# Optimization experiments

Hardware: AMD Instinct MI355X
Metric: run time of the kernel (lower is better)

The kernel has to match this reference:

```python
import jax, jax.numpy as jnp
import numpy as np

EPS = 1e-12


def _l2norm(x):
    # F.normalize(x, dim=1): x / max(||x||, eps)
    n = jnp.sqrt(jnp.sum(x * x, axis=1, keepdims=True))
    return x / jnp.maximum(n, EPS)


def _remove_diag(x):
    # x: [n, n] -> [n, n-1], dropping the diagonal (matches x[~eye].view(n, -1))
    n = x.shape[0]
    row = jnp.arange(n)[:, None]
    base = jnp.arange(n - 1)[None, :]
    cols = jnp.where(base < row, base, base + 1)  # column indices != row index
    return jnp.take_along_axis(x, cols, axis=1)


def _lid_mle(data, reference, k):
    # pairwise euclidean distances [n_data, n_ref]
    d2 = (jnp.sum(data * data, axis=1)[:, None]
          + jnp.sum(reference * reference, axis=1)[None, :]
          - 2.0 * data @ reference.T)
    dist = jnp.sqrt(jnp.maximum(d2, 0.0))
    # k+1 smallest distances (index 0 is the self-distance since data subset of reference)
    neg_top, _ = jax.lax.top_k(-dist, k + 1)
    d = -neg_top[:, 1:]  # [n, k], ascending, self excluded
    # MLE LID estimator: -k / sum_i log(d_i / d_k)
    return -k / jnp.sum(jnp.log(d / d[:, -1:] + EPS), axis=1)


def _byol_loss(p, z):
    z = jax.lax.stop_gradient(z)
    return 2.0 - 2.0 * jnp.sum(_l2norm(p) * _l2norm(z), axis=1)


def _track_logits(o0, o1):
    b = o0.shape[0]
    l00 = _remove_diag(jnp.einsum('nc,mc->nm', o0, o0))
    l01 = jnp.einsum('nc,mc->nm', o0, o1)
    l10 = jnp.einsum('nc,mc->nm', o1, o0)
    l11 = _remove_diag(jnp.einsum('nc,mc->nm', o1, o1))
    logits = jnp.concatenate([
        jnp.concatenate([l01, l00], axis=1),
        jnp.concatenate([l10, l11], axis=1)], axis=0)  # [2b, 2b-1]
    labels = jnp.tile(jnp.arange(b, dtype=jnp.int32), 2)
    return logits, labels


def setup_inputs() -> dict:
    key = jax.random.key(0)
    ks = jax.random.split(key, 9)
    B, Dfe, Dp, C = 4096, 2048, 256, 1000
    return {
        'fe_0': jax.random.normal(ks[0], (B, Dfe), jnp.float32),
        'fe_1': jax.random.normal(ks[1], (B, Dfe), jnp.float32),
        'p_0': jax.random.normal(ks[2], (B, Dp), jnp.float32),
        'p_1': jax.random.normal(ks[3], (B, Dp), jnp.float32),
        'z_0': jax.random.normal(ks[4], (B, Dp), jnp.float32),
        'z_1': jax.random.normal(ks[5], (B, Dp), jnp.float32),
        'cls_0': jax.random.normal(ks[6], (B, C), jnp.float32),
        'cls_1': jax.random.normal(ks[7], (B, C), jnp.float32),
        'online_labels': jax.random.randint(ks[8], (B,), 0, C, jnp.int32),
    }


def reference(fe_0, fe_1, p_0, p_1, z_0, z_1, cls_0, cls_1, online_labels):
    # BYOL symmetric loss
    main_loss = jnp.mean(_byol_loss(p_0, z_1) + _byol_loss(p_1, z_0))
    # online linear-probe cross-entropy on concatenated views
    cls = jnp.concatenate([cls_0, cls_1], axis=0)
    labels2 = jnp.concatenate([online_labels, online_labels], axis=0)
    logp = jax.nn.log_softmax(cls, axis=1)
    online_loss = -jnp.mean(jnp.take_along_axis(logp, labels2[:, None], axis=1)[:, 0])
    # LID tracking on backbone features (no-grad in original)
    fe = jnp.concatenate([fe_0, fe_1], axis=0)
    lids32 = _lid_mle(fe, fe, 32)
    lids512 = _lid_mle(fe, fe, 512)
    # contrastive-style logit tracking on normalized predictor outputs
    logits, labels = _track_logits(_l2norm(p_0), _l2norm(p_1))
    return main_loss, online_loss, logits, labels, lids32, lids512
```

## Files before the change

kernel.cpp:

```cpp
#include <hip/hip_runtime.h>
#include <math.h>

typedef __bf16 bf16;
typedef __bf16 bf16x8 __attribute__((ext_vector_type(8)));
typedef __bf16 bf16x4 __attribute__((ext_vector_type(4)));
typedef float f32x4 __attribute__((ext_vector_type(4)));

#define NROW 8192
#define BHALF 4096
#define DFE 2048
#define DP 256
#define NCLS 1000

#define LOGITS_N 8191
#define OUT_LOGITS 2
#define OUT_LABELS (2 + 8192 * 8191)
#define OUT_LIDS32 (OUT_LABELS + 8192)
#define OUT_LIDS512 (OUT_LIDS32 + 8192)

#define G0TILES 1056
#define G1TILES 2048

__device__ inline void gload16(const bf16* g, bf16* l) {
    __builtin_amdgcn_global_load_lds((const __attribute__((address_space(1))) void*)g,
                                     (__attribute__((address_space(3))) void*)l, 16, 0, 0);
}

__global__ __launch_bounds__(256) void init_kernel(float* out) {
    int i = blockIdx.x * 256 + threadIdx.x;
    if (i < 2) out[i] = 0.f;
    if (i < NROW) out[(size_t)OUT_LABELS + i] = (float)(i & (BHALF - 1));
}

__global__ __launch_bounds__(256) void split_fe_kernel(const float* __restrict__ fe0,
                                                       const float* __restrict__ fe1,
                                                       bf16* __restrict__ feh,
                                                       bf16* __restrict__ fel,
                                                       float* __restrict__ norms) {
    int row = blockIdx.x, tid = threadIdx.x;
    const float* src = (row < BHALF) ? fe0 + (size_t)row * DFE
                                     : fe1 + (size_t)(row - BHALF) * DFE;
    float ss = 0.f;
#pragma unroll
    for (int pass = 0; pass < 2; ++pass) {
        int c = (pass * 256 + tid) * 4;
        float4 v = *(const float4*)(src + c);
        ss += v.x * v.x + v.y * v.y + v.z * v.z + v.w * v.w;
        bf16 h0 = (bf16)v.x, h1 = (bf16)v.y, h2 = (bf16)v.z, h3 = (bf16)v.w;
        bf16 l0 = (bf16)(v.x - (float)h0), l1 = (bf16)(v.y - (float)h1);
        bf16 l2 = (bf16)(v.z - (float)h2), l3 = (bf16)(v.w - (float)h3);
        bf16x4 hv = {h0, h1, h2, h3};
        bf16x4 lv = {l0, l1, l2, l3};
        *(bf16x4*)(feh + (size_t)row * DFE + c) = hv;
        *(bf16x4*)(fel + (size_t)row * DFE + c) = lv;
    }
#pragma unroll
    for (int off = 32; off; off >>= 1) ss += __shfl_down(ss, off);
    __shared__ float red[4];
    if ((tid & 63) == 0) red[tid >> 6] = ss;
    __syncthreads();
    if (tid == 0) norms[row] = red[0] + red[1] + red[2] + red[3];
}

__global__ __launch_bounds__(256) void norm_split_p_kernel(const float* __restrict__ p0,
                                                           const float* __restrict__ p1,
                                                           bf16* __restrict__ oh) {
    int row = blockIdx.x, tid = threadIdx.x;
    const float* src = (row < BHALF) ? p0 + (size_t)row * DP
                                     : p1 + (size_t)(row - BHALF) * DP;
    float x = src[tid];
    float ss = x * x;
#pragma unroll
    for (int off = 32; off; off >>= 1) ss += __shfl_down(ss, off);
    __shared__ float red[4];
    if ((tid & 63) == 0) red[tid >> 6] = ss;
    __syncthreads();
    float tot = red[0] + red[1] + red[2] + red[3];
    float rn = 1.f / fmaxf(sqrtf(tot), 1e-12f);
    oh[(size_t)row * DP + tid] = (bf16)(x * rn);
}

__device__ inline float dot4(float4 a, float4 b) {
    return a.x * b.x + a.y * b.y + a.z * b.z + a.w * b.w;
}

__global__ __launch_bounds__(256) void byol_kernel(const float* __restrict__ p0,
                                                   const float* __restrict__ p1,
                                                   const float* __restrict__ z0,
                                                   const float* __restrict__ z1,
                                                   float* out) {
    int tid = threadIdx.x, wave = tid >> 6, lane = tid & 63;
    int row = blockIdx.x * 4 + wave;
    size_t base = (size_t)row * DP + lane * 4;
    float4 a0 = *(const float4*)(p0 + base);
    float4 b0 = *(const float4*)(z1 + base);
    float4 a1 = *(const float4*)(p1 + base);
    float4 b1 = *(const float4*)(z0 + base);
    float pp0 = dot4(a0, a0), zz0 = dot4(b0, b0), pz0 = dot4(a0, b0);
    float pp1 = dot4(a1, a1), zz1 = dot4(b1, b1), pz1 = dot4(a1, b1);
#pragma unroll
    for (int off = 32; off; off >>= 1) {
        pp0 += __shfl_down(pp0, off); zz0 += __shfl_down(zz0, off); pz0 += __shfl_down(pz0, off);
        pp1 += __shfl_down(pp1, off); zz1 += __shfl_down(zz1, off); pz1 += __shfl_down(pz1, off);
    }
    __shared__ float red[4];
    if (lane == 0) {
        float c0 = pz0 / (fmaxf(sqrtf(pp0), 1e-12f) * fmaxf(sqrtf(zz0), 1e-12f));
        float c1 = pz1 / (fmaxf(sqrtf(pp1), 1e-12f) * fmaxf(sqrtf(zz1), 1e-12f));
        red[wave] = (2.f - 2.f * c0) + (2.f - 2.f * c1);
    }
    __syncthreads();
    if (tid == 0) atomicAdd(out, (red[0] + red[1] + red[2] + red[3]) * (1.f / 4096.f));
}

__global__ __launch_bounds__(256) void online_kernel(const float* __restrict__ cls0,
                                                     const float* __restrict__ cls1,
                                                     const int* __restrict__ labels,
                                                     float* out) {
    int tid = threadIdx.x, wave = tid >> 6, lane = tid & 63;
    int row = blockIdx.x * 4 + wave;
    const float* src = (row < BHALF) ? cls0 + (size_t)row * NCLS
                                     : cls1 + (size_t)(row - BHALF) * NCLS;
    int lbl = labels[row & (BHALF - 1)];
    float xs[16];
    float mx = -INFINITY;
#pragma unroll
    for (int j = 0; j < 16; ++j) {
        int c = lane + j * 64;
        xs[j] = (c < NCLS) ? src[c] : -INFINITY;
        mx = fmaxf(mx, xs[j]);
    }
#pragma unroll
    for (int off = 32; off; off >>= 1) mx = fmaxf(mx, __shfl_xor(mx, off));
    float se = 0.f;
#pragma unroll
    for (int j = 0; j < 16; ++j) se += expf(xs[j] - mx);
#pragma unroll
    for (int off = 32; off; off >>= 1) se += __shfl_xor(se, off);
    __shared__ float red[4];
    if (lane == 0) red[wave] = src[lbl] - mx - logf(se);
    __syncthreads();
    if (tid == 0) atomicAdd(out + 1, -(red[0] + red[1] + red[2] + red[3]) * (1.f / 8192.f));
}

__global__ __launch_bounds__(512, 2) void gemm_kernel(const bf16* __restrict__ Hp,
                                                      const bf16* __restrict__ Lp,
                                                      const bf16* __restrict__ OHp,
                                                      const float* __restrict__ norms,
                                                      float* __restrict__ d2,
                                                      float* __restrict__ outlog) {
    __shared__ bf16 sm[2][24576];
    int tid = threadIdx.x, lane = tid & 63, wave = tid >> 6;
    int wr = wave >> 1, wc = wave & 1;
    int lrow = lane & 15, lquad = lane >> 4, r7 = lrow & 7, pg = lquad ^ r7;
    int rsub = lane >> 3, grp = lane & 7, lg = grp ^ rsub;

    int bid = blockIdx.x;
    int mode, tm, tn, ksh;
    const bf16 *Hmat, *Lmat;
    int Kd;
    if (bid < G0TILES) {
        mode = 0;
        int sw = (bid & 7) * (G0TILES / 8) + (bid >> 3);
        int i = 0;
        while ((i + 1) * (65 - (i + 1)) <= sw) ++i;
        tm = i;
        tn = 2 * i + (sw - i * (65 - i));
        Hmat = Hp; Lmat = Lp; Kd = DFE; ksh = 5;
    } else {
        mode = 1;
        int id = bid - G0TILES;
        int sw = (id & 7) * (G1TILES / 8) + (id >> 3);
        tm = sw & 31; tn = sw >> 5;
        Hmat = OHp; Lmat = OHp; Kd = DP; ksh = 2;
    }
    int NT = (mode == 0 ? 3 : 1) << ksh;
    int kmask = (1 << ksh) - 1;
    int arow0 = tm * 256, brow0 = tn * 128;
    size_t delta = (size_t)(Lmat - Hmat);

    const bf16* baseA[4];
    const bf16* baseB[2];
#pragma unroll
    for (int q = 0; q < 4; ++q)
        baseA[q] = Hmat + (size_t)(arow0 + q * 64 + wave * 8 + rsub) * Kd + lg * 8;
#pragma unroll
    for (int q = 0; q < 2; ++q)
        baseB[q] = Hmat + (size_t)(brow0 + q * 64 + wave * 8 + rsub) * Kd + lg * 8;

    int aoff[4], boff[4];
#pragma unroll
    for (int t = 0; t < 4; ++t) {
        aoff[t] = (((t * 4 + wr) * 16 + lrow) * 64) * 2 + pg * 16;
        boff[t] = 32768 + (((t * 2 + wc) * 16 + lrow) * 64) * 2 + pg * 16;
    }
    const char* S0 = (const char*)sm[0];
    const char* S1 = (const char*)sm[1];

    f32x4 acc[4][4];
    f32x4 zz = {0.f, 0.f, 0.f, 0.f};
#pragma unroll
    for (int i = 0; i < 4; ++i)
#pragma unroll
        for (int j = 0; j < 4; ++j) acc[i][j] = zz;

#define STAGE(nt, B)                                                        \
    do {                                                                    \
        int ch_ = (nt) >> ksh;                                              \
        int k_ = ((nt) & kmask) << 6;                                       \
        size_t dA_ = (ch_ == 1) ? delta : 0;                                \
        size_t dB_ = (ch_ == 2) ? delta : 0;                                \
        _Pragma("unroll") for (int q = 0; q < 4; ++q)                       \
            gload16(baseA[q] + dA_ + k_, (B) + q * 4096 + wave * 512);      \
        _Pragma("unroll") for (int q = 0; q < 2; ++q)                       \
            gload16(baseB[q] + dB_ + k_, (B) + 16384 + q * 4096 + wave * 512); \
    } while (0)

#define READF(AF, BF, SB)                                                   \
    do {                                                                    \
        _Pragma("unroll") for (int t = 0; t < 4; ++t) {                     \
            AF[t][0] = *(const bf16x8*)((SB) + aoff[t]);                    \
            AF[t][1] = *(const bf16x8*)((SB) + (aoff[t] ^ 64));             \
        }                                                                   \
        _Pragma("unroll") for (int t = 0; t < 4; ++t) {                     \
            BF[t][0] = *(const bf16x8*)((SB) + boff[t]);                    \
            BF[t][1] = *(const bf16x8*)((SB) + (boff[t] ^ 64));             \
        }                                                                   \
    } while (0)

#define MFMAC(AF, BF)                                                       \
    do {                                                                    \
        __builtin_amdgcn_s_setprio(1);                                      \
        _Pragma("unroll") for (int i = 0; i < 4; ++i)                       \
            _Pragma("unroll") for (int j = 0; j < 4; ++j) {                 \
                acc[i][j] = __builtin_amdgcn_mfma_f32_16x16x32_bf16(AF[i][0], BF[j][0], acc[i][j], 0, 0, 0); \
                acc[i][j] = __builtin_amdgcn_mfma_f32_16x16x32_bf16(AF[i][1], BF[j][1], acc[i][j], 0, 0, 0); \
            }                                                               \
        __builtin_amdgcn_s_setprio(0);                                      \
    } while (0)

    bf16x8 af0[4][2], bf0[4][2], af1[4][2], bf1[4][2];

    STAGE(0, sm[0]);
    STAGE(1, sm[1]);
    asm volatile("s_waitcnt vmcnt(6)" ::: "memory");
    __builtin_amdgcn_s_barrier();
    __builtin_amdgcn_sched_barrier(0);
    READF(af0, bf0, S0);

    for (int t = 0; t < NT; t += 2) {
        asm volatile("s_waitcnt lgkmcnt(0)" ::: "memory");
        __builtin_amdgcn_sched_barrier(0);
        __builtin_amdgcn_s_barrier();
        if (t + 2 < NT) {
            STAGE(t + 2, sm[0]);
            asm volatile("s_waitcnt vmcnt(6)" ::: "memory");
        } else {
            asm volatile("s_waitcnt vmcnt(0)" ::: "memory");
        }
        __builtin_amdgcn_s_barrier();
        __builtin_amdgcn_sched_barrier(0);
        READF(af1, bf1, S1);
        __builtin_amdgcn_sched_barrier(0);
        MFMAC(af0, bf0);

        asm volatile("s_waitcnt lgkmcnt(0)" ::: "memory");
        __builtin_amdgcn_sched_barrier(0);
        __builtin_amdgcn_s_barrier();
        if (t + 3 < NT) {
            STAGE(t + 3, sm[1]);
            asm volatile("s_waitcnt vmcnt(6)" ::: "memory");
        } else if (t + 2 < NT) {
            asm volatile("s_waitcnt vmcnt(0)" ::: "memory");
        }
        __builtin_amdgcn_s_barrier();
        if (t + 2 < NT) {
            __builtin_amdgcn_sched_barrier(0);
            READF(af0, bf0, S0);
            __builtin_amdgcn_sched_barrier(0);
        }
        MFMAC(af1, bf1);
    }

    if (mode == 0) {
#pragma unroll
        for (int i = 0; i < 4; ++i) {
#pragma unroll
            for (int e = 0; e < 4; ++e) {
                int grow = arow0 + (i * 4 + wr) * 16 + lquad * 4 + e;
                float na = norms[grow];
#pragma unroll
                for (int j = 0; j < 4; ++j) {
                    int gcol = tn * 128 + (j * 2 + wc) * 16 + lrow;
                    float v = na + norms[gcol] - 2.f * acc[i][j][e];
                    d2[(size_t)grow * NROW + gcol] = fmaxf(v, 0.f);
                }
            }
        }
    } else {
#pragma unroll
        for (int i = 0; i < 4; ++i) {
#pragma unroll
            for (int j = 0; j < 4; ++j) {
#pragma unroll
                for (int e = 0; e < 4; ++e) {
                    int r = arow0 + (i * 4 + wr) * 16 + lquad * 4 + e;
                    int c = tn * 128 + (j * 2 + wc) * 16 + lrow;
                    int oc = 0;
                    bool skip = false;
                    if (r < BHALF) {
                        if (c >= BHALF) oc = c - BHALF;
                        else if (c == r) skip = true;
                        else oc = BHALF + (c < r ? c : c - 1);
                    } else {
                        int rp = r - BHALF;
                        if (c < BHALF) oc = c;
                        else {
                            int cp = c - BHALF;
                            if (cp == rp) skip = true;
                            else oc = BHALF + (cp < rp ? cp : cp - 1);
                        }
                    }
                    if (!skip) outlog[(size_t)r * LOGITS_N + oc] = acc[i][j][e];
                }
            }
        }
    }
#undef STAGE
#undef READF
#undef MFMAC
}

__global__ __launch_bounds__(256) void mirror_kernel(float* __restrict__ d2) {
    int bj = blockIdx.x, bi = blockIdx.y;
    if (bi < bj) return;
    __shared__ float t[32][33];
    int tx = threadIdx.x & 31, ty = threadIdx.x >> 5;
#pragma unroll
    for (int r = 0; r < 32; r += 8)
        t[r + ty][tx] = d2[(size_t)(bj * 32 + r + ty) * NROW + bi * 32 + tx];
    __syncthreads();
#pragma unroll
    for (int r = 0; r < 32; r += 8) {
        int gi = bi * 32 + r + ty, gj = bj * 32 + tx;
        if (gi > gj) d2[(size_t)gi * NROW + gj] = t[tx][r + ty];
    }
}

__global__ __launch_bounds__(256) void select_kernel(const float* __restrict__ d2,
                                                     float* __restrict__ out) {
    int wave = threadIdx.x >> 6, lane = threadIdx.x & 63;
    int row = blockIdx.x * 4 + wave;
    const float4* drow4 = (const float4*)(d2 + (size_t)row * NROW);
    unsigned v[128];
    unsigned andv = 0xFFFFFFFFu, orv = 0u;
#pragma unroll
    for (int j = 0; j < 32; ++j) {
        int idx4 = j * 64 + lane;
        float4 f = drow4[idx4];
        int c0 = idx4 * 4;
        unsigned u0 = __float_as_uint(f.x), u1 = __float_as_uint(f.y);
        unsigned u2 = __float_as_uint(f.z), u3 = __float_as_uint(f.w);
        bool s0 = (c0 == row), s1 = (c0 + 1 == row), s2 = (c0 + 2 == row), s3 = (c0 + 3 == row);
        v[j * 4 + 0] = s0 ? 0xFFFFFFFFu : u0;
        v[j * 4 + 1] = s1 ? 0xFFFFFFFFu : u1;
        v[j * 4 + 2] = s2 ? 0xFFFFFFFFu : u2;
        v[j * 4 + 3] = s3 ? 0xFFFFFFFFu : u3;
        andv &= (s0 ? 0xFFFFFFFFu : u0); orv |= (s0 ? 0u : u0);
        andv &= (s1 ? 0xFFFFFFFFu : u1); orv |= (s1 ? 0u : u1);
        andv &= (s2 ? 0xFFFFFFFFu : u2); orv |= (s2 ? 0u : u2);
        andv &= (s3 ? 0xFFFFFFFFu : u3); orv |= (s3 ? 0u : u3);
    }
#pragma unroll
    for (int off = 32; off; off >>= 1) {
        andv &= __shfl_xor(andv, off);
        orv |= __shfl_xor(orv, off);
    }
    unsigned diff = andv ^ orv;
    int msb = 31 - __clz((int)(diff | 1u));
    unsigned common = (msb == 31) ? 0u : (andv & (0xFFFFFFFFu << (msb + 1)));
    unsigned p1 = common, p2 = common;
    for (int bit = msb; bit >= 0; --bit) {
        unsigned c1 = p1 | (1u << bit), c2 = p2 | (1u << bit);
        unsigned n1 = 0, n2 = 0;
#pragma unroll
        for (int j = 0; j < 128; ++j) { n1 += (v[j] < c1); n2 += (v[j] < c2); }
#pragma unroll
        for (int off = 32; off; off >>= 1) {
            n1 += __shfl_xor(n1, off);
            n2 += __shfl_xor(n2, off);
        }
        if (n1 < 32u) p1 = c1;
        if (n2 < 512u) p2 = c2;
    }
    float dk1 = sqrtf(__uint_as_float(p1));
    float dk2 = sqrtf(__uint_as_float(p2));
    float s1 = 0.f, s2 = 0.f;
#pragma unroll
    for (int j = 0; j < 128; ++j) {
        unsigned b = v[j];
        if (b < p2) {
            float d = sqrtf(__uint_as_float(b));
            s2 += logf(d / dk2 + 1e-12f);
            if (b < p1) s1 += logf(d / dk1 + 1e-12f);
        }
    }
#pragma unroll
    for (int off = 32; off; off >>= 1) {
        s1 += __shfl_xor(s1, off);
        s2 += __shfl_xor(s2, off);
    }
    if (lane == 0) {
        out[(size_t)OUT_LIDS32 + row] = -32.f / s1;
        out[(size_t)OUT_LIDS512 + row] = -512.f / s2;
    }
}

extern "C" void kernel_launch(void* const* d_in, const int* in_sizes, int n_in,
                              void* d_out, int out_size, void* d_ws, size_t ws_size,
                              hipStream_t stream) {
    const float* fe0 = (const float*)d_in[0];
    const float* fe1 = (const float*)d_in[1];
    const float* p0 = (const float*)d_in[2];
    const float* p1 = (const float*)d_in[3];
    const float* z0 = (const float*)d_in[4];
    const float* z1 = (const float*)d_in[5];
    const float* cls0 = (const float*)d_in[6];
    const float* cls1 = (const float*)d_in[7];
    const int* labels = (const int*)d_in[8];
    float* out = (float*)d_out;

    char* ws = (char*)d_ws;
    float* D2 = (float*)ws;
    bf16* FEH = (bf16*)(ws + 268435456UL);
    bf16* FEL = (bf16*)(ws + 268435456UL + 33554432UL);
    bf16* OH = (bf16*)(ws + 268435456UL + 2 * 33554432UL);
    float* NORMS = (float*)(ws + 268435456UL + 2 * 33554432UL + 4194304UL);

    init_kernel<<<32, 256, 0, stream>>>(out);
    split_fe_kernel<<<8192, 256, 0, stream>>>(fe0, fe1, FEH, FEL, NORMS);
    norm_split_p_kernel<<<8192, 256, 0, stream>>>(p0, p1, OH);
    byol_kernel<<<1024, 256, 0, stream>>>(p0, p1, z0, z1, out);
    online_kernel<<<2048, 256, 0, stream>>>(cls0, cls1, labels, out);
    gemm_kernel<<<G0TILES + G1TILES, 512, 0, stream>>>(FEH, FEL, OH, NORMS, D2, out + OUT_LOGITS);
    mirror_kernel<<<dim3(256, 256), 256, 0, stream>>>(D2);
    select_kernel<<<2048, 256, 0, stream>>>(D2, out);
}
```

Measured before the change: 1.252 ms.

## Enlarge GEMM tiles to 256x256 with quarter-phase pipelined staging; widen mirror tiles

```diff
diff --git a/kernel.cpp b/kernel.cpp
--- a/kernel.cpp
+++ b/kernel.cpp
@@ -18,8 +18,8 @@
 #define OUT_LIDS32 (OUT_LABELS + 8192)
 #define OUT_LIDS512 (OUT_LIDS32 + 8192)
 
-#define G0TILES 1056
-#define G1TILES 2048
+#define G0TILES 528
+#define G1TILES 1024
 
 __device__ inline void gload16(const bf16* g, bf16* l) {
     __builtin_amdgcn_global_load_lds((const __attribute__((address_space(1))) void*)g,
@@ -149,9 +149,9 @@
                                                       const float* __restrict__ norms,
                                                       float* __restrict__ d2,
                                                       float* __restrict__ outlog) {
-    __shared__ bf16 sm[2][24576];
+    __shared__ bf16 sm[2][32768];
     int tid = threadIdx.x, lane = tid & 63, wave = tid >> 6;
-    int wr = wave >> 1, wc = wave & 1;
+    int wr = wave >> 2, wn = wave & 3;
     int lrow = lane & 15, lquad = lane >> 4, r7 = lrow & 7, pg = lquad ^ r7;
     int rsub = lane >> 3, grp = lane & 7, lg = grp ^ rsub;
 
@@ -163,9 +163,9 @@
         mode = 0;
         int sw = (bid & 7) * (G0TILES / 8) + (bid >> 3);
         int i = 0;
-        while ((i + 1) * (65 - (i + 1)) <= sw) ++i;
+        while ((i + 1) * (64 - i) / 2 <= sw) ++i;
         tm = i;
-        tn = 2 * i + (sw - i * (65 - i));
+        tn = tm + (sw - i * (65 - i) / 2);
         Hmat = Hp; Lmat = Lp; Kd = DFE; ksh = 5;
     } else {
         mode = 1;
@@ -176,122 +176,147 @@
     }
     int NT = (mode == 0 ? 3 : 1) << ksh;
     int kmask = (1 << ksh) - 1;
-    int arow0 = tm * 256, brow0 = tn * 128;
+    int arow0 = tm * 256, brow0 = tn * 256;
     size_t delta = (size_t)(Lmat - Hmat);
 
-    const bf16* baseA[4];
-    const bf16* baseB[2];
-#pragma unroll
-    for (int q = 0; q < 4; ++q)
-        baseA[q] = Hmat + (size_t)(arow0 + q * 64 + wave * 8 + rsub) * Kd + lg * 8;
-#pragma unroll
-    for (int q = 0; q < 2; ++q)
-        baseB[q] = Hmat + (size_t)(brow0 + q * 64 + wave * 8 + rsub) * Kd + lg * 8;
-
-    int aoff[4], boff[4];
-#pragma unroll
-    for (int t = 0; t < 4; ++t) {
-        aoff[t] = (((t * 4 + wr) * 16 + lrow) * 64) * 2 + pg * 16;
-        boff[t] = 32768 + (((t * 2 + wc) * 16 + lrow) * 64) * 2 + pg * 16;
-    }
-    const char* S0 = (const char*)sm[0];
-    const char* S1 = (const char*)sm[1];
-
-    f32x4 acc[4][4];
+    const bf16* baseA0 = Hmat + (size_t)(arow0 + wave * 8 + rsub) * Kd + lg * 8;
+    const bf16* baseB0 = Hmat + (size_t)(brow0 + wave * 8 + rsub) * Kd + lg * 8;
+
+    int aoffbase[2], boffbase[2];
+    aoffbase[0] = (wr * 64 + lrow) * 128 + pg * 16;
+    aoffbase[1] = aoffbase[0] + 128 * 128;
+    boffbase[0] = 32768 + (wn * 32 + lrow) * 128 + pg * 16;
+    boffbase[1] = boffbase[0] + 128 * 128;
+
+    f32x4 acc[8][4];
     f32x4 zz = {0.f, 0.f, 0.f, 0.f};
 #pragma unroll
-    for (int i = 0; i < 4; ++i)
+    for (int i = 0; i < 8; ++i)
 #pragma unroll
         for (int j = 0; j < 4; ++j) acc[i][j] = zz;
 
-#define STAGE(nt, B)                                                        \
-    do {                                                                    \
-        int ch_ = (nt) >> ksh;                                              \
-        int k_ = ((nt) & kmask) << 6;                                       \
-        size_t dA_ = (ch_ == 1) ? delta : 0;                                \
-        size_t dB_ = (ch_ == 2) ? delta : 0;                                \
-        _Pragma("unroll") for (int q = 0; q < 4; ++q)                       \
-            gload16(baseA[q] + dA_ + k_, (B) + q * 4096 + wave * 512);      \
-        _Pragma("unroll") for (int q = 0; q < 2; ++q)                       \
-            gload16(baseB[q] + dB_ + k_, (B) + 16384 + q * 4096 + wave * 512); \
-    } while (0)
-
-#define READF(AF, BF, SB)                                                   \
-    do {                                                                    \
-        _Pragma("unroll") for (int t = 0; t < 4; ++t) {                     \
-            AF[t][0] = *(const bf16x8*)((SB) + aoff[t]);                    \
-            AF[t][1] = *(const bf16x8*)((SB) + (aoff[t] ^ 64));             \
-        }                                                                   \
-        _Pragma("unroll") for (int t = 0; t < 4; ++t) {                     \
-            BF[t][0] = *(const bf16x8*)((SB) + boff[t]);                    \
-            BF[t][1] = *(const bf16x8*)((SB) + (boff[t] ^ 64));             \
-        }                                                                   \
-    } while (0)
-
-#define MFMAC(AF, BF)                                                       \
-    do {                                                                    \
-        __builtin_amdgcn_s_setprio(1);                                      \
-        _Pragma("unroll") for (int i = 0; i < 4; ++i)                       \
-            _Pragma("unroll") for (int j = 0; j < 4; ++j) {                 \
-                acc[i][j] = __builtin_amdgcn_mfma_f32_16x16x32_bf16(AF[i][0], BF[j][0], acc[i][j], 0, 0, 0); \
-                acc[i][j] = __builtin_amdgcn_mfma_f32_16x16x32_bf16(AF[i][1], BF[j][1], acc[i][j], 0, 0, 0); \
-            }                                                               \
-        __builtin_amdgcn_s_setprio(0);                                      \
-    } while (0)
-
-    bf16x8 af0[4][2], bf0[4][2], af1[4][2], bf1[4][2];
-
-    STAGE(0, sm[0]);
-    STAGE(1, sm[1]);
-    asm volatile("s_waitcnt vmcnt(6)" ::: "memory");
+#define STAGE_A(tau, h, dstbuf)                                                   \
+    do {                                                                          \
+        int tau_ = (tau);                                                         \
+        if (tau_ < NT) {                                                          \
+            int ch_ = tau_ >> ksh;                                                \
+            size_t dd_ = (ch_ == 1) ? delta : 0;                                  \
+            int k_ = (tau_ & kmask) << 6;                                         \
+            bf16* d_ = (dstbuf) + (h) * 8192 + wave * 512;                        \
+            gload16(baseA0 + (size_t)((h) * 128) * Kd + dd_ + k_, d_);            \
+            gload16(baseA0 + (size_t)((h) * 128 + 64) * Kd + dd_ + k_, d_ + 4096);\
+        }                                                                         \
+    } while (0)
+
+#define STAGE_B(tau, h, dstbuf)                                                   \
+    do {                                                                          \
+        int tau_ = (tau);                                                         \
+        if (tau_ < NT) {                                                          \
+            int ch_ = tau_ >> ksh;                                                \
+            size_t dd_ = (ch_ == 2) ? delta : 0;                                  \
+            int k_ = (tau_ & kmask) << 6;                                         \
+            bf16* d_ = (dstbuf) + 16384 + (h) * 8192 + wave * 512;                \
+            gload16(baseB0 + (size_t)((h) * 128) * Kd + dd_ + k_, d_);            \
+            gload16(baseB0 + (size_t)((h) * 128 + 64) * Kd + dd_ + k_, d_ + 4096);\
+        }                                                                         \
+    } while (0)
+
+#define READ_A(AF, MI)                                                            \
+    do {                                                                          \
+        _Pragma("unroll") for (int f = 0; f < 4; ++f) {                           \
+            int off_ = aoffbase[(MI)] + f * 2048;                                 \
+            AF[f][0] = *(const bf16x8*)(Sb + off_);                               \
+            AF[f][1] = *(const bf16x8*)(Sb + (off_ ^ 64));                        \
+        }                                                                         \
+    } while (0)
+
+#define READ_B(BF, NI)                                                            \
+    do {                                                                          \
+        _Pragma("unroll") for (int jj = 0; jj < 2; ++jj) {                        \
+            int off_ = boffbase[(NI)] + jj * 2048;                                \
+            BF[jj][0] = *(const bf16x8*)(Sb + off_);                              \
+            BF[jj][1] = *(const bf16x8*)(Sb + (off_ ^ 64));                       \
+        }                                                                         \
+    } while (0)
+
+#define MFMA_PHASE(MI, NI, AF, BF)                                                \
+    do {                                                                          \
+        __builtin_amdgcn_s_setprio(1);                                            \
+        _Pragma("unroll") for (int f = 0; f < 4; ++f)                             \
+            _Pragma("unroll") for (int jj = 0; jj < 2; ++jj) {                    \
+                acc[(MI)*4 + f][(NI)*2 + jj] = __builtin_amdgcn_mfma_f32_16x16x32_bf16( \
+                    AF[f][0], BF[jj][0], acc[(MI)*4 + f][(NI)*2 + jj], 0, 0, 0);  \
+                acc[(MI)*4 + f][(NI)*2 + jj] = __builtin_amdgcn_mfma_f32_16x16x32_bf16( \
+                    AF[f][1], BF[jj][1], acc[(MI)*4 + f][(NI)*2 + jj], 0, 0, 0);  \
+            }                                                                     \
+        __builtin_amdgcn_s_setprio(0);                                            \
+    } while (0)
+
+#define VM_END(tailflag)                                                          \
+    do {                                                                          \
+        if (tailflag) asm volatile("s_waitcnt vmcnt(0)" ::: "memory");            \
+        else          asm volatile("s_waitcnt vmcnt(10)" ::: "memory");           \
+    } while (0)
+
+    bf16x8 af[4][2], b0f[2][2], b1f[2][2];
+
+    STAGE_A(0, 0, sm[0]); STAGE_B(0, 0, sm[0]); STAGE_B(0, 1, sm[0]); STAGE_A(0, 1, sm[0]);
+    STAGE_A(1, 0, sm[1]); STAGE_B(1, 0, sm[1]); STAGE_B(1, 1, sm[1]);
+    asm volatile("s_waitcnt vmcnt(10)" ::: "memory");
     __builtin_amdgcn_s_barrier();
-    __builtin_amdgcn_sched_barrier(0);
-    READF(af0, bf0, S0);
-
-    for (int t = 0; t < NT; t += 2) {
+
+    for (int t = 0; t < NT; ++t) {
+        const char* Sb = (const char*)sm[t & 1];
+        bf16* samebuf = sm[t & 1];
+        bf16* otherbuf = sm[(t + 1) & 1];
+        bool tail = (t >= NT - 3);
+
+        READ_A(af, 0);
+        READ_B(b0f, 0);
+        STAGE_A(t + 1, 1, otherbuf);
+        __builtin_amdgcn_s_barrier();
         asm volatile("s_waitcnt lgkmcnt(0)" ::: "memory");
         __builtin_amdgcn_sched_barrier(0);
-        __builtin_amdgcn_s_barrier();
-        if (t + 2 < NT) {
-            STAGE(t + 2, sm[0]);
-            asm volatile("s_waitcnt vmcnt(6)" ::: "memory");
-        } else {
-            asm volatile("s_waitcnt vmcnt(0)" ::: "memory");
-        }
-        __builtin_amdgcn_s_barrier();
-        __builtin_amdgcn_sched_barrier(0);
-        READF(af1, bf1, S1);
-        __builtin_amdgcn_sched_barrier(0);
-        MFMAC(af0, bf0);
-
+        MFMA_PHASE(0, 0, af, b0f);
+        VM_END(tail);
+        __builtin_amdgcn_s_barrier();
+
+        READ_B(b1f, 1);
+        STAGE_A(t + 2, 0, samebuf);
+        __builtin_amdgcn_s_barrier();
         asm volatile("s_waitcnt lgkmcnt(0)" ::: "memory");
         __builtin_amdgcn_sched_barrier(0);
-        __builtin_amdgcn_s_barrier();
-        if (t + 3 < NT) {
-            STAGE(t + 3, sm[1]);
-            asm volatile("s_waitcnt vmcnt(6)" ::: "memory");
-        } else if (t + 2 < NT) {
-            asm volatile("s_waitcnt vmcnt(0)" ::: "memory");
-        }
-        __builtin_amdgcn_s_barrier();
-        if (t + 2 < NT) {
-            __builtin_amdgcn_sched_barrier(0);
-            READF(af0, bf0, S0);
-            __builtin_amdgcn_sched_barrier(0);
-        }
-        MFMAC(af1, bf1);
+        MFMA_PHASE(0, 1, af, b1f);
+        VM_END(tail);
+        __builtin_amdgcn_s_barrier();
+
+        READ_A(af, 1);
+        STAGE_B(t + 2, 0, samebuf);
+        __builtin_amdgcn_s_barrier();
+        asm volatile("s_waitcnt lgkmcnt(0)" ::: "memory");
+        __builtin_amdgcn_sched_barrier(0);
+        MFMA_PHASE(1, 0, af, b0f);
+        if (tail) asm volatile("s_waitcnt vmcnt(0)" ::: "memory");
+        __builtin_amdgcn_s_barrier();
+
+        STAGE_B(t + 2, 1, samebuf);
+        __builtin_amdgcn_s_barrier();
+        __builtin_amdgcn_sched_barrier(0);
+        MFMA_PHASE(1, 1, af, b1f);
+        VM_END(tail);
+        __builtin_amdgcn_s_barrier();
     }
 
     if (mode == 0) {
 #pragma unroll
-        for (int i = 0; i < 4; ++i) {
+        for (int i = 0; i < 8; ++i) {
 #pragma unroll
             for (int e = 0; e < 4; ++e) {
-                int grow = arow0 + (i * 4 + wr) * 16 + lquad * 4 + e;
+                int grow = arow0 + (i >> 2) * 128 + wr * 64 + (i & 3) * 16 + lquad * 4 + e;
                 float na = norms[grow];
 #pragma unroll
                 for (int j = 0; j < 4; ++j) {
-                    int gcol = tn * 128 + (j * 2 + wc) * 16 + lrow;
+                    int gcol = brow0 + (j >> 1) * 128 + wn * 32 + (j & 1) * 16 + lrow;
                     float v = na + norms[gcol] - 2.f * acc[i][j][e];
                     d2[(size_t)grow * NROW + gcol] = fmaxf(v, 0.f);
                 }
@@ -299,13 +324,13 @@
         }
     } else {
 #pragma unroll
-        for (int i = 0; i < 4; ++i) {
+        for (int i = 0; i < 8; ++i) {
 #pragma unroll
             for (int j = 0; j < 4; ++j) {
 #pragma unroll
                 for (int e = 0; e < 4; ++e) {
-                    int r = arow0 + (i * 4 + wr) * 16 + lquad * 4 + e;
-                    int c = tn * 128 + (j * 2 + wc) * 16 + lrow;
+                    int r = arow0 + (i >> 2) * 128 + wr * 64 + (i & 3) * 16 + lquad * 4 + e;
+                    int c = brow0 + (j >> 1) * 128 + wn * 32 + (j & 1) * 16 + lrow;
                     int oc = 0;
                     bool skip = false;
                     if (r < BHALF) {
@@ -326,23 +351,26 @@
             }
         }
     }
-#undef STAGE
-#undef READF
-#undef MFMAC
+#undef STAGE_A
+#undef STAGE_B
+#undef READ_A
+#undef READ_B
+#undef MFMA_PHASE
+#undef VM_END
 }
 
 __global__ __launch_bounds__(256) void mirror_kernel(float* __restrict__ d2) {
     int bj = blockIdx.x, bi = blockIdx.y;
     if (bi < bj) return;
-    __shared__ float t[32][33];
-    int tx = threadIdx.x & 31, ty = threadIdx.x >> 5;
-#pragma unroll
-    for (int r = 0; r < 32; r += 8)
-        t[r + ty][tx] = d2[(size_t)(bj * 32 + r + ty) * NROW + bi * 32 + tx];
+    __shared__ float t[64][65];
+    int tx = threadIdx.x & 63, ty = threadIdx.x >> 6;
+#pragma unroll
+    for (int r = 0; r < 64; r += 4)
+        t[r + ty][tx] = d2[(size_t)(bj * 64 + r + ty) * NROW + bi * 64 + tx];
     __syncthreads();
 #pragma unroll
-    for (int r = 0; r < 32; r += 8) {
-        int gi = bi * 32 + r + ty, gj = bj * 32 + tx;
+    for (int r = 0; r < 64; r += 4) {
+        int gi = bi * 64 + r + ty, gj = bj * 64 + tx;
         if (gi > gj) d2[(size_t)gi * NROW + gj] = t[tx][r + ty];
     }
 }
@@ -443,6 +471,6 @@
     byol_kernel<<<1024, 256, 0, stream>>>(p0, p1, z0, z1, out);
     online_kernel<<<2048, 256, 0, stream>>>(cls0, cls1, labels, out);
     gemm_kernel<<<G0TILES + G1TILES, 512, 0, stream>>>(FEH, FEL, OH, NORMS, D2, out + OUT_LOGITS);
-    mirror_kernel<<<dim3(256, 256), 256, 0, stream>>>(D2);
+    mirror_kernel<<<dim3(128, 128), 256, 0, stream>>>(D2);
     select_kernel<<<2048, 256, 0, stream>>>(D2, out);
 }
```

Result: slower. 1.292 ms (+3.2%).
